# Optimization experiments

Hardware: AMD Instinct MI355X
Metric: run time of the kernel (lower is better)

Reference implementation:

```python
import jax, jax.numpy as jnp
import numpy as np

D_MODEL = 1024
N_HEADS = 16
D_HEAD = D_MODEL // N_HEADS


def setup_inputs() -> dict:
    key = jax.random.key(0)
    ks = jax.random.split(key, 9)
    s = 1.0 / np.sqrt(D_MODEL)
    x = jax.random.normal(ks[0], (2, 2048, D_MODEL), dtype=jnp.float32)
    # torch nn.Linear stores weight [out, in]; we store [in, out] for x @ W
    Wq = jax.random.uniform(ks[1], (D_MODEL, D_MODEL), jnp.float32, -s, s)
    bq = jax.random.uniform(ks[2], (D_MODEL,), jnp.float32, -s, s)
    Wk = jax.random.uniform(ks[3], (D_MODEL, D_MODEL), jnp.float32, -s, s)
    bk = jax.random.uniform(ks[4], (D_MODEL,), jnp.float32, -s, s)
    Wv = jax.random.uniform(ks[5], (D_MODEL, D_MODEL), jnp.float32, -s, s)
    bv = jax.random.uniform(ks[6], (D_MODEL,), jnp.float32, -s, s)
    Wo = jax.random.uniform(ks[7], (D_MODEL, D_MODEL), jnp.float32, -s, s)
    bo = jax.random.uniform(ks[8], (D_MODEL,), jnp.float32, -s, s)
    return {"x": x, "Wq": Wq, "bq": bq, "Wk": Wk, "bk": bk,
            "Wv": Wv, "bv": bv, "Wo": Wo, "bo": bo}


def reference(x, Wq, bq, Wk, bk, Wv, bv, Wo, bo):
    B, S, _ = x.shape
    # project and split heads: [B, H, S, Dh]
    def split(t):
        return t.reshape(B, S, N_HEADS, D_HEAD).transpose(0, 2, 1, 3)
    Q = split(x @ Wq + bq)
    K = split(x @ Wk + bk)
    V = split(x @ Wv + bv)
    scale = 1.0 / jnp.sqrt(jnp.asarray(D_HEAD, x.dtype))
    scores = jnp.einsum('bhqd,bhkd->bhqk', Q, K) * scale  # [B,H,S,S]
    attn = jax.nn.softmax(scores, axis=-1)
    out = jnp.einsum('bhqk,bhkd->bhqd', attn, V)  # [B,H,S,Dh]
    out = out.transpose(0, 2, 1, 3).reshape(B, S, D_MODEL)
    return out @ Wo + bo
```

## Files before the change

### kernel.cpp

```cpp
#include <hip/hip_runtime.h>
#include <hip/hip_bf16.h>
#include <cmath>

#define D_MODEL 1024
#define N_HEADS 16
#define D_HEAD  64
#define BATCH   2
#define SEQ     2048
#define M_TOT   (BATCH*SEQ)

typedef __attribute__((ext_vector_type(8))) short short8;
typedef __attribute__((ext_vector_type(4))) float f32x4;

static __device__ __forceinline__ ushort f2bf(float f) {
    __hip_bfloat16 h = __float2bfloat16(f);
    return *reinterpret_cast<ushort*>(&h);
}

static __device__ __forceinline__ void gload_lds16(const void* g, void* l) {
    __builtin_amdgcn_global_load_lds((const __attribute__((address_space(1))) unsigned*)g,
                                     (__attribute__((address_space(3))) unsigned*)l,
                                     16, 0, 0);
}

__global__ __launch_bounds__(256)
void f32_to_bf16_kernel(const float* __restrict__ in, ushort* __restrict__ out, int n4)
{
    const int i = blockIdx.x * 256 + threadIdx.x;
    if (i < n4) {
        const float4 v = ((const float4*)in)[i];
        ushort4 u;
        u.x = f2bf(v.x); u.y = f2bf(v.y); u.z = f2bf(v.z); u.w = f2bf(v.w);
        ((ushort4*)out)[i] = u;
    }
}

__global__ __launch_bounds__(256)
void transpose_w4_kernel(const float* __restrict__ W0, const float* __restrict__ W1,
                         const float* __restrict__ W2, const float* __restrict__ W3,
                         ushort* __restrict__ Wt0)
{
    __shared__ float Ts[64][65];
    const int z = blockIdx.z;
    const float* W = (z == 0) ? W0 : (z == 1) ? W1 : (z == 2) ? W2 : W3;
    ushort* Wt = Wt0 + (size_t)z * D_MODEL * D_MODEL;

    const int t  = threadIdx.x;
    const int n0 = blockIdx.x * 64;
    const int k0 = blockIdx.y * 64;
    const int rr = t >> 4;
    const int c4 = (t & 15) * 4;

#pragma unroll
    for (int i = 0; i < 4; ++i) {
        const int r = rr + i * 16;
        const float4 v = *(const float4*)&W[(size_t)(k0 + r) * D_MODEL + n0 + c4];
        Ts[r][c4 + 0] = v.x; Ts[r][c4 + 1] = v.y;
        Ts[r][c4 + 2] = v.z; Ts[r][c4 + 3] = v.w;
    }
    __syncthreads();
#pragma unroll
    for (int i = 0; i < 4; ++i) {
        const int nn = rr + i * 16;
        ushort4 u;
        u.x = f2bf(Ts[c4 + 0][nn]); u.y = f2bf(Ts[c4 + 1][nn]);
        u.z = f2bf(Ts[c4 + 2][nn]); u.w = f2bf(Ts[c4 + 3][nn]);
        *(ushort4*)&Wt[(size_t)(n0 + nn) * D_MODEL + k0 + c4] = u;
    }
}

__global__ __launch_bounds__(256)
void transpose_v_kernel(const ushort* __restrict__ V, ushort* __restrict__ Vt)
{
    __shared__ ushort Ts[64][68];
    const int t  = threadIdx.x;
    const int s0 = blockIdx.x * 64;
    const int bh = blockIdx.y;
    const int rr = t >> 4;
    const int c4 = (t & 15) * 4;

#pragma unroll
    for (int i = 0; i < 4; ++i) {
        const int r = rr + i * 16;
        const ushort4 v = *(const ushort4*)&V[((size_t)bh * SEQ + s0 + r) * D_HEAD + c4];
        Ts[r][c4 + 0] = v.x; Ts[r][c4 + 1] = v.y;
        Ts[r][c4 + 2] = v.z; Ts[r][c4 + 3] = v.w;
    }
    __syncthreads();
#pragma unroll
    for (int i = 0; i < 4; ++i) {
        const int dh = rr + i * 16;
        ushort4 u;
        u.x = Ts[c4 + 0][dh]; u.y = Ts[c4 + 1][dh];
        u.z = Ts[c4 + 2][dh]; u.w = Ts[c4 + 3][dh];
        *(ushort4*)&Vt[((size_t)bh * D_HEAD + dh) * SEQ + s0 + c4] = u;
    }
}

__global__ __launch_bounds__(256)
void gemm_qkv_mfma(const ushort* __restrict__ A, const ushort* __restrict__ Bt,
                   const float* __restrict__ bq, const float* __restrict__ bk,
                   const float* __restrict__ bv, ushort* __restrict__ QKV)
{
    __shared__ ushort As[128 * 64];
    __shared__ ushort Bs[128 * 64];

    const int t    = threadIdx.x;
    const int lane = t & 63;
    const int w    = t >> 6;
    const int wr   = w >> 1;
    const int wc   = w & 1;
    const int l16  = lane & 15;
    const int g    = lane >> 4;
    const int m0   = blockIdx.y * 128;
    const int n0   = blockIdx.x * 128;

    f32x4 acc[4][4];
#pragma unroll
    for (int i = 0; i < 4; ++i)
#pragma unroll
        for (int j = 0; j < 4; ++j) acc[i][j] = f32x4{0.f, 0.f, 0.f, 0.f};

    for (int kt = 0; kt < D_MODEL; kt += 64) {
        __syncthreads();
        const ushort* Ag = A  + (size_t)m0 * D_MODEL + kt;
        const ushort* Bg = Bt + (size_t)n0 * D_MODEL + kt;
#pragma unroll
        for (int it = 0; it < 4; ++it) {
            const int b   = (it * 256 + t) * 16;
            const int row = b >> 7;
            const int src = (b & 127) ^ ((row & 7) << 4);
            const int lof = (it * 256 + (t & ~63)) * 8;
            gload_lds16(Ag + (size_t)row * D_MODEL + (src >> 1), As + lof);
            gload_lds16(Bg + (size_t)row * D_MODEL + (src >> 1), Bs + lof);
        }
        __syncthreads();

#pragma unroll
        for (int kh = 0; kh < 2; ++kh) {
            short8 a[4], bfr[4];
#pragma unroll
            for (int fm = 0; fm < 4; ++fm) {
                const int row  = wr * 64 + fm * 16 + l16;
                const int byte = row * 128 + (((kh << 6) | (g << 4)) ^ ((row & 7) << 4));
                a[fm] = *(const short8*)((const char*)As + byte);
            }
#pragma unroll
            for (int fn = 0; fn < 4; ++fn) {
                const int row  = wc * 64 + fn * 16 + l16;
                const int byte = row * 128 + (((kh << 6) | (g << 4)) ^ ((row & 7) << 4));
                bfr[fn] = *(const short8*)((const char*)Bs + byte);
            }
#pragma unroll
            for (int fm = 0; fm < 4; ++fm)
#pragma unroll
                for (int fn = 0; fn < 4; ++fn)
                    acc[fm][fn] = __builtin_amdgcn_mfma_f32_16x16x32_bf16(a[fm], bfr[fn], acc[fm][fn], 0, 0, 0);
        }
    }

#pragma unroll
    for (int fm = 0; fm < 4; ++fm) {
        const int mb = m0 + wr * 64 + fm * 16 + g * 4;
#pragma unroll
        for (int fn = 0; fn < 4; ++fn) {
            const int n    = n0 + wc * 64 + fn * 16 + l16;
            const int proj = n >> 10;
            const int nn   = n & 1023;
            const float bn = (proj == 0) ? bq[nn] : (proj == 1) ? bk[nn] : bv[nn];
            const float sc = (proj == 0) ? 0.125f : 1.0f;
            ushort* outp = QKV + (size_t)proj * M_TOT * D_MODEL;
#pragma unroll
            for (int r = 0; r < 4; ++r) {
                const float c = (acc[fm][fn][r] + bn) * sc;
                const int m  = mb + r;
                const int bb = m >> 11;
                const int s  = m & (SEQ - 1);
                const int h  = nn >> 6;
                const int dh = nn & 63;
                outp[(((size_t)(bb * N_HEADS + h)) * SEQ + s) * D_HEAD + dh] = f2bf(c);
            }
        }
    }
}

__global__ __launch_bounds__(256)
void gemm_out_mfma(const ushort* __restrict__ A, const ushort* __restrict__ Bt,
                   const float* __restrict__ bias, float* __restrict__ outp)
{
    __shared__ ushort As[128 * 64];
    __shared__ ushort Bs[128 * 64];

    const int t    = threadIdx.x;
    const int lane = t & 63;
    const int w    = t >> 6;
    const int wr   = w >> 1;
    const int wc   = w & 1;
    const int l16  = lane & 15;
    const int g    = lane >> 4;
    const int m0   = blockIdx.y * 128;
    const int n0   = blockIdx.x * 128;

    f32x4 acc[4][4];
#pragma unroll
    for (int i = 0; i < 4; ++i)
#pragma unroll
        for (int j = 0; j < 4; ++j) acc[i][j] = f32x4{0.f, 0.f, 0.f, 0.f};

    for (int kt = 0; kt < D_MODEL; kt += 64) {
        __syncthreads();
        const ushort* Ag = A  + (size_t)m0 * D_MODEL + kt;
        const ushort* Bg = Bt + (size_t)n0 * D_MODEL + kt;
#pragma unroll
        for (int it = 0; it < 4; ++it) {
            const int b   = (it * 256 + t) * 16;
            const int row = b >> 7;
            const int src = (b & 127) ^ ((row & 7) << 4);
            const int lof = (it * 256 + (t & ~63)) * 8;
            gload_lds16(Ag + (size_t)row * D_MODEL + (src >> 1), As + lof);
            gload_lds16(Bg + (size_t)row * D_MODEL + (src >> 1), Bs + lof);
        }
        __syncthreads();

#pragma unroll
        for (int kh = 0; kh < 2; ++kh) {
            short8 a[4], bfr[4];
#pragma unroll
            for (int fm = 0; fm < 4; ++fm) {
                const int row  = wr * 64 + fm * 16 + l16;
                const int byte = row * 128 + (((kh << 6) | (g << 4)) ^ ((row & 7) << 4));
                a[fm] = *(const short8*)((const char*)As + byte);
            }
#pragma unroll
            for (int fn = 0; fn < 4; ++fn) {
                const int row  = wc * 64 + fn * 16 + l16;
                const int byte = row * 128 + (((kh << 6) | (g << 4)) ^ ((row & 7) << 4));
                bfr[fn] = *(const short8*)((const char*)Bs + byte);
            }
#pragma unroll
            for (int fm = 0; fm < 4; ++fm)
#pragma unroll
                for (int fn = 0; fn < 4; ++fn)
                    acc[fm][fn] = __builtin_amdgcn_mfma_f32_16x16x32_bf16(a[fm], bfr[fn], acc[fm][fn], 0, 0, 0);
        }
    }

#pragma unroll
    for (int fm = 0; fm < 4; ++fm) {
        const int mb = m0 + wr * 64 + fm * 16 + g * 4;
#pragma unroll
        for (int fn = 0; fn < 4; ++fn) {
            const int n  = n0 + wc * 64 + fn * 16 + l16;
            const float bn = bias[n];
#pragma unroll
            for (int r = 0; r < 4; ++r)
                outp[(size_t)(mb + r) * D_MODEL + n] = acc[fm][fn][r] + bn;
        }
    }
}

__global__ __launch_bounds__(256)
void flash_attn_mfma(const ushort* __restrict__ Q, const ushort* __restrict__ K,
                     const ushort* __restrict__ Vt, ushort* __restrict__ AO)
{
    __shared__ ushort Kl[2][64 * 64];
    __shared__ ushort Vl[2][64 * 64];
    __shared__ ushort Ps[4][2][16][80];

    const int t    = threadIdx.x;
    const int w    = t >> 6;
    const int lane = t & 63;
    const int l16  = lane & 15;
    const int g    = lane >> 4;
    const int qt   = blockIdx.x;
    const int bh   = blockIdx.y;

    const size_t qkbase = (size_t)bh * SEQ * D_HEAD;
    const ushort* Vg0 = Vt + (size_t)bh * D_HEAD * SEQ;

    short8 qf[2][2];
#pragma unroll
    for (int tt = 0; tt < 2; ++tt) {
        const int q0 = qt * 128 + w * 32 + tt * 16;
        const ushort* qp = Q + qkbase + (size_t)(q0 + l16) * D_HEAD + g * 8;
        qf[tt][0] = *(const short8*)(qp);
        qf[tt][1] = *(const short8*)(qp + 32);
    }

    f32x4 o[2][4];
    float m_r[2], l_r[2];
#pragma unroll
    for (int tt = 0; tt < 2; ++tt) {
        m_r[tt] = -INFINITY; l_r[tt] = 0.f;
#pragma unroll
        for (int d = 0; d < 4; ++d) o[tt][d] = f32x4{0.f, 0.f, 0.f, 0.f};
    }

    auto stage = [&](int ktile, int b) {
        const ushort* Kg = K + qkbase + (size_t)(ktile * 64) * D_HEAD;
        const ushort* Vg = Vg0 + ktile * 64;
#pragma unroll
        for (int it = 0; it < 2; ++it) {
            const int bb  = (it * 256 + t) * 16;
            const int row = bb >> 7;
            const int src = (bb & 127) ^ ((row & 7) << 4);
            const int lof = (it * 256 + (t & ~63)) * 8;
            gload_lds16(Kg + (size_t)row * D_HEAD + (src >> 1), &Kl[b][lof]);
            gload_lds16(Vg + (size_t)row * SEQ + (src >> 1), &Vl[b][lof]);
        }
    };

    stage(0, 0);
    __syncthreads();

    const int NT = SEQ / 64;
    for (int kt = 0; kt < NT; ++kt) {
        const int buf = kt & 1;
        if (kt + 1 < NT) stage(kt + 1, buf ^ 1);

        short8 kf[4][2];
#pragma unroll
        for (int nt = 0; nt < 4; ++nt) {
            const int row = nt * 16 + l16;
#pragma unroll
            for (int ks = 0; ks < 2; ++ks) {
                const int byte = row * 128 + (((ks * 64) | (g * 16)) ^ ((row & 7) << 4));
                kf[nt][ks] = *(const short8*)((const char*)&Kl[buf][0] + byte);
            }
        }

        f32x4 st[2][4];
#pragma unroll
        for (int tt = 0; tt < 2; ++tt)
#pragma unroll
            for (int nt = 0; nt < 4; ++nt) {
                f32x4 a = f32x4{0.f, 0.f, 0.f, 0.f};
                a = __builtin_amdgcn_mfma_f32_16x16x32_bf16(kf[nt][0], qf[tt][0], a, 0, 0, 0);
                a = __builtin_amdgcn_mfma_f32_16x16x32_bf16(kf[nt][1], qf[tt][1], a, 0, 0, 0);
                st[tt][nt] = a;
            }

#pragma unroll
        for (int tt = 0; tt < 2; ++tt) {
            float pmax = st[tt][0][0];
#pragma unroll
            for (int nt = 0; nt < 4; ++nt)
#pragma unroll
                for (int r = 0; r < 4; ++r) pmax = fmaxf(pmax, st[tt][nt][r]);
            pmax = fmaxf(pmax, __shfl_xor(pmax, 16, 64));
            pmax = fmaxf(pmax, __shfl_xor(pmax, 32, 64));

            if (__any(pmax - m_r[tt] > 8.f)) {
                const float mnew  = fmaxf(m_r[tt], pmax);
                const float alpha = __expf(m_r[tt] - mnew);
                m_r[tt] = mnew;
                l_r[tt] *= alpha;
                float ar[4];
#pragma unroll
                for (int r = 0; r < 4; ++r) ar[r] = __shfl(alpha, g * 4 + r, 64);
#pragma unroll
                for (int dt = 0; dt < 4; ++dt)
#pragma unroll
                    for (int r = 0; r < 4; ++r) o[tt][dt][r] *= ar[r];
            }

            float rs = 0.f;
#pragma unroll
            for (int nt = 0; nt < 4; ++nt) {
                ushort4 pk;
#pragma unroll
                for (int r = 0; r < 4; ++r) {
                    const float p = __expf(st[tt][nt][r] - m_r[tt]);
                    rs += p;
                    ((ushort*)&pk)[r] = f2bf(p);
                }
                *(ushort4*)&Ps[w][tt][l16][nt * 16 + g * 4] = pk;
            }
            rs += __shfl_xor(rs, 16, 64);
            rs += __shfl_xor(rs, 32, 64);
            l_r[tt] += rs;
        }

        short8 vf[4][2];
#pragma unroll
        for (int dt = 0; dt < 4; ++dt) {
            const int row = dt * 16 + l16;
#pragma unroll
            for (int ks = 0; ks < 2; ++ks) {
                const int byte = row * 128 + (((ks * 64) | (g * 16)) ^ ((row & 7) << 4));
                vf[dt][ks] = *(const short8*)((const char*)&Vl[buf][0] + byte);
            }
        }

#pragma unroll
        for (int tt = 0; tt < 2; ++tt)
#pragma unroll
            for (int ks = 0; ks < 2; ++ks) {
                const short8 pf = *(const short8*)&Ps[w][tt][l16][ks * 32 + g * 8];
#pragma unroll
                for (int dt = 0; dt < 4; ++dt)
                    o[tt][dt] = __builtin_amdgcn_mfma_f32_16x16x32_bf16(pf, vf[dt][ks], o[tt][dt], 0, 0, 0);
            }

        __syncthreads();
    }

    const int b = bh >> 4;
    const int h = bh & 15;
#pragma unroll
    for (int tt = 0; tt < 2; ++tt) {
        const int q0 = qt * 128 + w * 32 + tt * 16;
        float lr_row[4];
#pragma unroll
        for (int r = 0; r < 4; ++r) lr_row[r] = __shfl(l_r[tt], g * 4 + r, 64);
#pragma unroll
        for (int r = 0; r < 4; ++r) {
            const float inv = 1.f / lr_row[r];
            const size_t row = (size_t)b * SEQ + q0 + g * 4 + r;
#pragma unroll
            for (int dt = 0; dt < 4; ++dt)
                AO[row * D_MODEL + h * D_HEAD + dt * 16 + l16] = f2bf(o[tt][dt][r] * inv);
        }
    }
}

extern "C" void kernel_launch(void* const* d_in, const int* in_sizes, int n_in,
                              void* d_out, int out_size, void* d_ws, size_t ws_size,
                              hipStream_t stream)
{
    const float* x  = (const float*)d_in[0];
    const float* Wq = (const float*)d_in[1];
    const float* bq = (const float*)d_in[2];
    const float* Wk = (const float*)d_in[3];
    const float* bk = (const float*)d_in[4];
    const float* Wv = (const float*)d_in[5];
    const float* bv = (const float*)d_in[6];
    const float* Wo = (const float*)d_in[7];
    const float* bo = (const float*)d_in[8];
    float* out = (float*)d_out;

    const size_t NELT = (size_t)M_TOT * D_MODEL;
    const size_t WELT = (size_t)D_MODEL * D_MODEL;
    ushort* xb  = (ushort*)d_ws;
    ushort* Wqt = xb + NELT;
    ushort* Wot = Wqt + 3 * WELT;
    ushort* Qb  = xb + 2 * NELT;
    ushort* Vb  = xb + 4 * NELT;
    ushort* Vtb = xb;
    ushort* AOb = Vb;

    f32_to_bf16_kernel<<<dim3((M_TOT * D_MODEL / 4 + 255) / 256), 256, 0, stream>>>(x, xb, M_TOT * D_MODEL / 4);
    transpose_w4_kernel<<<dim3(D_MODEL / 64, D_MODEL / 64, 4), 256, 0, stream>>>(Wq, Wk, Wv, Wo, Wqt);
    gemm_qkv_mfma<<<dim3(3 * D_MODEL / 128, M_TOT / 128), 256, 0, stream>>>(xb, Wqt, bq, bk, bv, Qb);
    transpose_v_kernel<<<dim3(SEQ / 64, BATCH * N_HEADS), 256, 0, stream>>>(Vb, Vtb);
    flash_attn_mfma<<<dim3(SEQ / 128, BATCH * N_HEADS), 256, 0, stream>>>(Qb, Qb + NELT, Vtb, AOb);
    gemm_out_mfma<<<dim3(D_MODEL / 128, M_TOT / 128), 256, 0, stream>>>(AOb, Wot, bo, out);
}
```

Baseline: 149.2 us.

## Split attention over KV halves, fuse V transpose into QKV GEMM, use exp2

```diff
diff --git a/kernel.cpp b/kernel.cpp
--- a/kernel.cpp
+++ b/kernel.cpp
@@ -8,13 +8,19 @@
 #define BATCH   2
 #define SEQ     2048
 #define M_TOT   (BATCH*SEQ)
+#define NELT    ((size_t)M_TOT * D_MODEL)
 
 typedef __attribute__((ext_vector_type(8))) short short8;
 typedef __attribute__((ext_vector_type(4))) float f32x4;
+
+#define QSCALE (0.125f * 1.44269504088896f)
 
 static __device__ __forceinline__ ushort f2bf(float f) {
     __hip_bfloat16 h = __float2bfloat16(f);
     return *reinterpret_cast<ushort*>(&h);
+}
+static __device__ __forceinline__ float bf2f(short u) {
+    return __uint_as_float(((unsigned)(ushort)u) << 16);
 }
 
 static __device__ __forceinline__ void gload_lds16(const void* g, void* l) {
@@ -66,34 +72,6 @@
         u.x = f2bf(Ts[c4 + 0][nn]); u.y = f2bf(Ts[c4 + 1][nn]);
         u.z = f2bf(Ts[c4 + 2][nn]); u.w = f2bf(Ts[c4 + 3][nn]);
         *(ushort4*)&Wt[(size_t)(n0 + nn) * D_MODEL + k0 + c4] = u;
-    }
-}
-
-__global__ __launch_bounds__(256)
-void transpose_v_kernel(const ushort* __restrict__ V, ushort* __restrict__ Vt)
-{
-    __shared__ ushort Ts[64][68];
-    const int t  = threadIdx.x;
-    const int s0 = blockIdx.x * 64;
-    const int bh = blockIdx.y;
-    const int rr = t >> 4;
-    const int c4 = (t & 15) * 4;
-
-#pragma unroll
-    for (int i = 0; i < 4; ++i) {
-        const int r = rr + i * 16;
-        const ushort4 v = *(const ushort4*)&V[((size_t)bh * SEQ + s0 + r) * D_HEAD + c4];
-        Ts[r][c4 + 0] = v.x; Ts[r][c4 + 1] = v.y;
-        Ts[r][c4 + 2] = v.z; Ts[r][c4 + 3] = v.w;
-    }
-    __syncthreads();
-#pragma unroll
-    for (int i = 0; i < 4; ++i) {
-        const int dh = rr + i * 16;
-        ushort4 u;
-        u.x = Ts[c4 + 0][dh]; u.y = Ts[c4 + 1][dh];
-        u.z = Ts[c4 + 2][dh]; u.w = Ts[c4 + 3][dh];
-        *(ushort4*)&Vt[((size_t)bh * D_HEAD + dh) * SEQ + s0 + c4] = u;
     }
 }
 
@@ -161,24 +139,33 @@
 
 #pragma unroll
     for (int fm = 0; fm < 4; ++fm) {
-        const int mb = m0 + wr * 64 + fm * 16 + g * 4;
+        const int mb  = m0 + wr * 64 + fm * 16 + g * 4;
+        const int bb  = mb >> 11;
+        const int sA  = mb & (SEQ - 1);
 #pragma unroll
         for (int fn = 0; fn < 4; ++fn) {
             const int n    = n0 + wc * 64 + fn * 16 + l16;
             const int proj = n >> 10;
             const int nn   = n & 1023;
+            const int h    = nn >> 6;
+            const int dh   = nn & 63;
             const float bn = (proj == 0) ? bq[nn] : (proj == 1) ? bk[nn] : bv[nn];
-            const float sc = (proj == 0) ? 0.125f : 1.0f;
-            ushort* outp = QKV + (size_t)proj * M_TOT * D_MODEL;
-#pragma unroll
-            for (int r = 0; r < 4; ++r) {
-                const float c = (acc[fm][fn][r] + bn) * sc;
-                const int m  = mb + r;
-                const int bb = m >> 11;
-                const int s  = m & (SEQ - 1);
-                const int h  = nn >> 6;
-                const int dh = nn & 63;
-                outp[(((size_t)(bb * N_HEADS + h)) * SEQ + s) * D_HEAD + dh] = f2bf(c);
+            if (proj == 2) {
+                ushort4 pk;
+                pk.x = f2bf(acc[fm][fn][0] + bn);
+                pk.y = f2bf(acc[fm][fn][1] + bn);
+                pk.z = f2bf(acc[fm][fn][2] + bn);
+                pk.w = f2bf(acc[fm][fn][3] + bn);
+                *(ushort4*)&QKV[2 * NELT +
+                                (((size_t)(bb * N_HEADS + h)) * D_HEAD + dh) * SEQ + sA] = pk;
+            } else {
+                const float sc = (proj == 0) ? QSCALE : 1.0f;
+                ushort* outp = QKV + (size_t)proj * NELT;
+#pragma unroll
+                for (int r = 0; r < 4; ++r) {
+                    const float c = (acc[fm][fn][r] + bn) * sc;
+                    outp[(((size_t)(bb * N_HEADS + h)) * SEQ + sA + r) * D_HEAD + dh] = f2bf(c);
+                }
             }
         }
     }
@@ -260,8 +247,9 @@
 }
 
 __global__ __launch_bounds__(256)
-void flash_attn_mfma(const ushort* __restrict__ Q, const ushort* __restrict__ K,
-                     const ushort* __restrict__ Vt, ushort* __restrict__ AO)
+void flash_attn_split(const ushort* __restrict__ Q, const ushort* __restrict__ K,
+                      const ushort* __restrict__ Vt, ushort* __restrict__ Opart,
+                      float2* __restrict__ ML)
 {
     __shared__ ushort Kl[2][64 * 64];
     __shared__ ushort Vl[2][64 * 64];
@@ -272,7 +260,8 @@
     const int lane = t & 63;
     const int l16  = lane & 15;
     const int g    = lane >> 4;
-    const int qt   = blockIdx.x;
+    const int hv   = blockIdx.x & 1;
+    const int qt   = blockIdx.x >> 1;
     const int bh   = blockIdx.y;
 
     const size_t qkbase = (size_t)bh * SEQ * D_HEAD;
@@ -310,13 +299,13 @@
         }
     };
 
-    stage(0, 0);
+    const int it0 = hv * 16;
+    stage(it0, 0);
     __syncthreads();
 
-    const int NT = SEQ / 64;
-    for (int kt = 0; kt < NT; ++kt) {
-        const int buf = kt & 1;
-        if (kt + 1 < NT) stage(kt + 1, buf ^ 1);
+    for (int it = 0; it < 16; ++it) {
+        const int buf = it & 1;
+        if (it + 1 < 16) stage(it0 + it + 1, buf ^ 1);
 
         short8 kf[4][2];
 #pragma unroll
@@ -330,6 +319,7 @@
         }
 
         f32x4 st[2][4];
+        __builtin_amdgcn_s_setprio(1);
 #pragma unroll
         for (int tt = 0; tt < 2; ++tt)
 #pragma unroll
@@ -339,6 +329,7 @@
                 a = __builtin_amdgcn_mfma_f32_16x16x32_bf16(kf[nt][1], qf[tt][1], a, 0, 0, 0);
                 st[tt][nt] = a;
             }
+        __builtin_amdgcn_s_setprio(0);
 
 #pragma unroll
         for (int tt = 0; tt < 2; ++tt) {
@@ -352,7 +343,7 @@
 
             if (__any(pmax - m_r[tt] > 8.f)) {
                 const float mnew  = fmaxf(m_r[tt], pmax);
-                const float alpha = __expf(m_r[tt] - mnew);
+                const float alpha = exp2f(m_r[tt] - mnew);
                 m_r[tt] = mnew;
                 l_r[tt] *= alpha;
                 float ar[4];
@@ -370,7 +361,7 @@
                 ushort4 pk;
 #pragma unroll
                 for (int r = 0; r < 4; ++r) {
-                    const float p = __expf(st[tt][nt][r] - m_r[tt]);
+                    const float p = exp2f(st[tt][nt][r] - m_r[tt]);
                     rs += p;
                     ((ushort*)&pk)[r] = f2bf(p);
                 }
@@ -392,6 +383,7 @@
             }
         }
 
+        __builtin_amdgcn_s_setprio(1);
 #pragma unroll
         for (int tt = 0; tt < 2; ++tt)
 #pragma unroll
@@ -401,12 +393,11 @@
                 for (int dt = 0; dt < 4; ++dt)
                     o[tt][dt] = __builtin_amdgcn_mfma_f32_16x16x32_bf16(pf, vf[dt][ks], o[tt][dt], 0, 0, 0);
             }
+        __builtin_amdgcn_s_setprio(0);
 
         __syncthreads();
     }
 
-    const int b = bh >> 4;
-    const int h = bh & 15;
 #pragma unroll
     for (int tt = 0; tt < 2; ++tt) {
         const int q0 = qt * 128 + w * 32 + tt * 16;
@@ -416,12 +407,48 @@
 #pragma unroll
         for (int r = 0; r < 4; ++r) {
             const float inv = 1.f / lr_row[r];
-            const size_t row = (size_t)b * SEQ + q0 + g * 4 + r;
+            const size_t row = (size_t)bh * SEQ + q0 + g * 4 + r;
 #pragma unroll
             for (int dt = 0; dt < 4; ++dt)
-                AO[row * D_MODEL + h * D_HEAD + dt * 16 + l16] = f2bf(o[tt][dt][r] * inv);
-        }
-    }
+                Opart[(size_t)hv * NELT + row * D_HEAD + dt * 16 + l16] =
+                    f2bf(o[tt][dt][r] * inv);
+        }
+        if (g == 0)
+            ML[(size_t)hv * BATCH * N_HEADS * SEQ + (size_t)bh * SEQ + q0 + l16] =
+                make_float2(m_r[tt], l_r[tt]);
+    }
+}
+
+__global__ __launch_bounds__(256)
+void merge_attn(const ushort* __restrict__ Opart, const float2* __restrict__ ML,
+                ushort* __restrict__ AO)
+{
+    const int idx = blockIdx.x * 256 + threadIdx.x;
+    const int dh8 = idx & 7;
+    const int s   = (idx >> 3) & (SEQ - 1);
+    const int bh  = idx >> 14;
+    const size_t rowh = (size_t)bh * SEQ + s;
+
+    const float2 ml1 = ML[rowh];
+    const float2 ml2 = ML[(size_t)BATCH * N_HEADS * SEQ + rowh];
+    const float m   = fmaxf(ml1.x, ml2.x);
+    const float c1  = ml1.y * exp2f(ml1.x - m);
+    const float c2  = ml2.y * exp2f(ml2.x - m);
+    const float inv = 1.f / (c1 + c2);
+    const float w1  = c1 * inv;
+    const float w2  = c2 * inv;
+
+    const size_t off = rowh * D_HEAD + dh8 * 8;
+    const short8 o1 = *(const short8*)&Opart[off];
+    const short8 o2 = *(const short8*)&Opart[NELT + off];
+    short8 res;
+#pragma unroll
+    for (int j = 0; j < 8; ++j)
+        res[j] = (short)f2bf(w1 * bf2f(o1[j]) + w2 * bf2f(o2[j]));
+
+    const int b = bh >> 4;
+    const int h = bh & 15;
+    *(short8*)&AO[((size_t)b * SEQ + s) * D_MODEL + h * D_HEAD + dh8 * 8] = res;
 }
 
 extern "C" void kernel_launch(void* const* d_in, const int* in_sizes, int n_in,
@@ -439,20 +466,21 @@
     const float* bo = (const float*)d_in[8];
     float* out = (float*)d_out;
 
-    const size_t NELT = (size_t)M_TOT * D_MODEL;
     const size_t WELT = (size_t)D_MODEL * D_MODEL;
-    ushort* xb  = (ushort*)d_ws;
-    ushort* Wqt = xb + NELT;
-    ushort* Wot = Wqt + 3 * WELT;
-    ushort* Qb  = xb + 2 * NELT;
-    ushort* Vb  = xb + 4 * NELT;
-    ushort* Vtb = xb;
-    ushort* AOb = Vb;
-
-    f32_to_bf16_kernel<<<dim3((M_TOT * D_MODEL / 4 + 255) / 256), 256, 0, stream>>>(x, xb, M_TOT * D_MODEL / 4);
+    ushort* xb    = (ushort*)d_ws;
+    ushort* Wqt   = xb + NELT;
+    ushort* Wot   = Wqt + 3 * WELT;
+    ushort* Qb    = xb + 2 * NELT;
+    ushort* Kb    = Qb + NELT;
+    ushort* Vtb   = Kb + NELT;
+    ushort* Opart = xb + 5 * NELT;
+    float2* ML    = (float2*)(xb + 7 * NELT);
+    ushort* AOb   = xb;
+
+    f32_to_bf16_kernel<<<dim3(M_TOT * D_MODEL / 4 / 256), 256, 0, stream>>>(x, xb, M_TOT * D_MODEL / 4);
     transpose_w4_kernel<<<dim3(D_MODEL / 64, D_MODEL / 64, 4), 256, 0, stream>>>(Wq, Wk, Wv, Wo, Wqt);
     gemm_qkv_mfma<<<dim3(3 * D_MODEL / 128, M_TOT / 128), 256, 0, stream>>>(xb, Wqt, bq, bk, bv, Qb);
-    transpose_v_kernel<<<dim3(SEQ / 64, BATCH * N_HEADS), 256, 0, stream>>>(Vb, Vtb);
-    flash_attn_mfma<<<dim3(SEQ / 128, BATCH * N_HEADS), 256, 0, stream>>>(Qb, Qb + NELT, Vtb, AOb);
+    flash_attn_split<<<dim3(2 * SEQ / 128, BATCH * N_HEADS), 256, 0, stream>>>(Qb, Kb, Vtb, Opart, ML);
+    merge_attn<<<dim3(BATCH * N_HEADS * SEQ * 8 / 256), 256, 0, stream>>>(Opart, ML, AOb);
     gemm_out_mfma<<<dim3(D_MODEL / 128, M_TOT / 128), 256, 0, stream>>>(AOb, Wot, bo, out);
 }
```

After: 166.7 us. 1.12x slower.

## Fuse V transpose into QKV epilogue, use exp2 softmax, swizzle P tile, set priorities

Applied to the files above, without the earlier changes.

```diff
diff --git a/kernel.cpp b/kernel.cpp
--- a/kernel.cpp
+++ b/kernel.cpp
@@ -8,9 +8,12 @@
 #define BATCH   2
 #define SEQ     2048
 #define M_TOT   (BATCH*SEQ)
+#define NELT    ((size_t)M_TOT * D_MODEL)
 
 typedef __attribute__((ext_vector_type(8))) short short8;
 typedef __attribute__((ext_vector_type(4))) float f32x4;
+
+#define QSCALE (0.125f * 1.44269504088896f)
 
 static __device__ __forceinline__ ushort f2bf(float f) {
     __hip_bfloat16 h = __float2bfloat16(f);
@@ -66,34 +69,6 @@
         u.x = f2bf(Ts[c4 + 0][nn]); u.y = f2bf(Ts[c4 + 1][nn]);
         u.z = f2bf(Ts[c4 + 2][nn]); u.w = f2bf(Ts[c4 + 3][nn]);
         *(ushort4*)&Wt[(size_t)(n0 + nn) * D_MODEL + k0 + c4] = u;
-    }
-}
-
-__global__ __launch_bounds__(256)
-void transpose_v_kernel(const ushort* __restrict__ V, ushort* __restrict__ Vt)
-{
-    __shared__ ushort Ts[64][68];
-    const int t  = threadIdx.x;
-    const int s0 = blockIdx.x * 64;
-    const int bh = blockIdx.y;
-    const int rr = t >> 4;
-    const int c4 = (t & 15) * 4;
-
-#pragma unroll
-    for (int i = 0; i < 4; ++i) {
-        const int r = rr + i * 16;
-        const ushort4 v = *(const ushort4*)&V[((size_t)bh * SEQ + s0 + r) * D_HEAD + c4];
-        Ts[r][c4 + 0] = v.x; Ts[r][c4 + 1] = v.y;
-        Ts[r][c4 + 2] = v.z; Ts[r][c4 + 3] = v.w;
-    }
-    __syncthreads();
-#pragma unroll
-    for (int i = 0; i < 4; ++i) {
-        const int dh = rr + i * 16;
-        ushort4 u;
-        u.x = Ts[c4 + 0][dh]; u.y = Ts[c4 + 1][dh];
-        u.z = Ts[c4 + 2][dh]; u.w = Ts[c4 + 3][dh];
-        *(ushort4*)&Vt[((size_t)bh * D_HEAD + dh) * SEQ + s0 + c4] = u;
     }
 }
 
@@ -161,24 +136,33 @@
 
 #pragma unroll
     for (int fm = 0; fm < 4; ++fm) {
-        const int mb = m0 + wr * 64 + fm * 16 + g * 4;
+        const int mb  = m0 + wr * 64 + fm * 16 + g * 4;
+        const int bb  = mb >> 11;
+        const int sA  = mb & (SEQ - 1);
 #pragma unroll
         for (int fn = 0; fn < 4; ++fn) {
             const int n    = n0 + wc * 64 + fn * 16 + l16;
             const int proj = n >> 10;
             const int nn   = n & 1023;
+            const int h    = nn >> 6;
+            const int dh   = nn & 63;
             const float bn = (proj == 0) ? bq[nn] : (proj == 1) ? bk[nn] : bv[nn];
-            const float sc = (proj == 0) ? 0.125f : 1.0f;
-            ushort* outp = QKV + (size_t)proj * M_TOT * D_MODEL;
-#pragma unroll
-            for (int r = 0; r < 4; ++r) {
-                const float c = (acc[fm][fn][r] + bn) * sc;
-                const int m  = mb + r;
-                const int bb = m >> 11;
-                const int s  = m & (SEQ - 1);
-                const int h  = nn >> 6;
-                const int dh = nn & 63;
-                outp[(((size_t)(bb * N_HEADS + h)) * SEQ + s) * D_HEAD + dh] = f2bf(c);
+            if (proj == 2) {
+                ushort4 pk;
+                pk.x = f2bf(acc[fm][fn][0] + bn);
+                pk.y = f2bf(acc[fm][fn][1] + bn);
+                pk.z = f2bf(acc[fm][fn][2] + bn);
+                pk.w = f2bf(acc[fm][fn][3] + bn);
+                *(ushort4*)&QKV[2 * NELT +
+                                (((size_t)(bb * N_HEADS + h)) * D_HEAD + dh) * SEQ + sA] = pk;
+            } else {
+                const float sc = (proj == 0) ? QSCALE : 1.0f;
+                ushort* outp = QKV + (size_t)proj * NELT;
+#pragma unroll
+                for (int r = 0; r < 4; ++r) {
+                    const float c = (acc[fm][fn][r] + bn) * sc;
+                    outp[(((size_t)(bb * N_HEADS + h)) * SEQ + sA + r) * D_HEAD + dh] = f2bf(c);
+                }
             }
         }
     }
@@ -265,7 +249,7 @@
 {
     __shared__ ushort Kl[2][64 * 64];
     __shared__ ushort Vl[2][64 * 64];
-    __shared__ ushort Ps[4][2][16][80];
+    __shared__ ushort Ps[4][2][16][64];
 
     const int t    = threadIdx.x;
     const int w    = t >> 6;
@@ -330,6 +314,7 @@
         }
 
         f32x4 st[2][4];
+        __builtin_amdgcn_s_setprio(1);
 #pragma unroll
         for (int tt = 0; tt < 2; ++tt)
 #pragma unroll
@@ -339,6 +324,7 @@
                 a = __builtin_amdgcn_mfma_f32_16x16x32_bf16(kf[nt][1], qf[tt][1], a, 0, 0, 0);
                 st[tt][nt] = a;
             }
+        __builtin_amdgcn_s_setprio(0);
 
 #pragma unroll
         for (int tt = 0; tt < 2; ++tt) {
@@ -352,7 +338,7 @@
 
             if (__any(pmax - m_r[tt] > 8.f)) {
                 const float mnew  = fmaxf(m_r[tt], pmax);
-                const float alpha = __expf(m_r[tt] - mnew);
+                const float alpha = exp2f(m_r[tt] - mnew);
                 m_r[tt] = mnew;
                 l_r[tt] *= alpha;
                 float ar[4];
@@ -370,11 +356,12 @@
                 ushort4 pk;
 #pragma unroll
                 for (int r = 0; r < 4; ++r) {
-                    const float p = __expf(st[tt][nt][r] - m_r[tt]);
+                    const float p = exp2f(st[tt][nt][r] - m_r[tt]);
                     rs += p;
                     ((ushort*)&pk)[r] = f2bf(p);
                 }
-                *(ushort4*)&Ps[w][tt][l16][nt * 16 + g * 4] = pk;
+                const int pb = (nt * 32 + g * 8) ^ ((l16 & 7) << 4);
+                *(ushort4*)((char*)&Ps[w][tt][0][0] + l16 * 128 + pb) = pk;
             }
             rs += __shfl_xor(rs, 16, 64);
             rs += __shfl_xor(rs, 32, 64);
@@ -392,15 +379,18 @@
             }
         }
 
+        __builtin_amdgcn_s_setprio(1);
 #pragma unroll
         for (int tt = 0; tt < 2; ++tt)
 #pragma unroll
             for (int ks = 0; ks < 2; ++ks) {
-                const short8 pf = *(const short8*)&Ps[w][tt][l16][ks * 32 + g * 8];
+                const int rb = (ks * 64 + g * 16) ^ ((l16 & 7) << 4);
+                const short8 pf = *(const short8*)((const char*)&Ps[w][tt][0][0] + l16 * 128 + rb);
 #pragma unroll
                 for (int dt = 0; dt < 4; ++dt)
                     o[tt][dt] = __builtin_amdgcn_mfma_f32_16x16x32_bf16(pf, vf[dt][ks], o[tt][dt], 0, 0, 0);
             }
+        __builtin_amdgcn_s_setprio(0);
 
         __syncthreads();
     }
@@ -439,20 +429,18 @@
     const float* bo = (const float*)d_in[8];
     float* out = (float*)d_out;
 
-    const size_t NELT = (size_t)M_TOT * D_MODEL;
     const size_t WELT = (size_t)D_MODEL * D_MODEL;
     ushort* xb  = (ushort*)d_ws;
     ushort* Wqt = xb + NELT;
     ushort* Wot = Wqt + 3 * WELT;
     ushort* Qb  = xb + 2 * NELT;
-    ushort* Vb  = xb + 4 * NELT;
-    ushort* Vtb = xb;
-    ushort* AOb = Vb;
-
-    f32_to_bf16_kernel<<<dim3((M_TOT * D_MODEL / 4 + 255) / 256), 256, 0, stream>>>(x, xb, M_TOT * D_MODEL / 4);
+    ushort* Kb  = Qb + NELT;
+    ushort* Vtb = Kb + NELT;
+    ushort* AOb = xb + 5 * NELT;
+
+    f32_to_bf16_kernel<<<dim3(M_TOT * D_MODEL / 4 / 256), 256, 0, stream>>>(x, xb, M_TOT * D_MODEL / 4);
     transpose_w4_kernel<<<dim3(D_MODEL / 64, D_MODEL / 64, 4), 256, 0, stream>>>(Wq, Wk, Wv, Wo, Wqt);
     gemm_qkv_mfma<<<dim3(3 * D_MODEL / 128, M_TOT / 128), 256, 0, stream>>>(xb, Wqt, bq, bk, bv, Qb);
-    transpose_v_kernel<<<dim3(SEQ / 64, BATCH * N_HEADS), 256, 0, stream>>>(Vb, Vtb);
-    flash_attn_mfma<<<dim3(SEQ / 128, BATCH * N_HEADS), 256, 0, stream>>>(Qb, Qb + NELT, Vtb, AOb);
+    flash_attn_mfma<<<dim3(SEQ / 128, BATCH * N_HEADS), 256, 0, stream>>>(Qb, Kb, Vtb, AOb);
     gemm_out_mfma<<<dim3(D_MODEL / 128, M_TOT / 128), 256, 0, stream>>>(AOb, Wot, bo, out);
 }
```

After: 156.0 us. 1.05x slower.
